# Kernel optimization log

Measured on AMD Instinct MI355X. Metric: run time of the kernel, lower is better.

The kernel has to match this reference:

```python
import jax, jax.numpy as jnp
import numpy as np

B, S, E = 2, 2048, 2048
H, D = 16, 128           # n_heads, head_dim (= rope_dim)
BASE = 10000.0


def _rope_tables(seq_len, dim):
    inv_freq = 1.0 / (BASE ** (jnp.arange(0, dim, 2, dtype=jnp.float32) / dim))
    t = jnp.arange(seq_len, dtype=jnp.float32)
    freqs = jnp.outer(t, inv_freq)                 # [S, D/2]
    emb = jnp.concatenate([freqs, freqs], axis=-1)  # [S, D]
    cos = jnp.cos(emb)[None, :, None, :]            # [1, S, 1, D]
    sin = jnp.sin(emb)[None, :, None, :]
    return cos, sin


def _rotate_half(x):
    x1, x2 = x[..., : x.shape[-1] // 2], x[..., x.shape[-1] // 2:]
    return jnp.concatenate([-x2, x1], axis=-1)


def setup_inputs() -> dict:
    key = jax.random.key(0)
    ks = jax.random.split(key, 9)
    s = 1.0 / np.sqrt(E)
    return {
        "x": jax.random.normal(ks[0], (B, S, E), dtype=jnp.float32),
        "Wq": jax.random.uniform(ks[1], (E, E), jnp.float32, -s, s),
        "bq": jax.random.uniform(ks[2], (E,), jnp.float32, -s, s),
        "Wk": jax.random.uniform(ks[3], (E, E), jnp.float32, -s, s),
        "bk": jax.random.uniform(ks[4], (E,), jnp.float32, -s, s),
        "Wv": jax.random.uniform(ks[5], (E, E), jnp.float32, -s, s),
        "bv": jax.random.uniform(ks[6], (E,), jnp.float32, -s, s),
        "Wp": jax.random.uniform(ks[7], (E, E), jnp.float32, -s, s),
        "bp": jax.random.uniform(ks[8], (E,), jnp.float32, -s, s),
    }


def reference(x, Wq, bq, Wk, bk, Wv, bv, Wp, bp):
    b, s, e = x.shape
    # QKV projections (torch Linear: y = x W^T + b)
    q = (jnp.einsum("bse,fe->bsf", x, Wq) + bq).reshape(b, s, H, D)
    k = (jnp.einsum("bse,fe->bsf", x, Wk) + bk).reshape(b, s, H, D)
    v = (jnp.einsum("bse,fe->bsf", x, Wv) + bv).reshape(b, s, H, D)
    # RoPE (rope_dim == head_dim, start_pos = 0)
    cos, sin = _rope_tables(s, D)
    q = q * cos + _rotate_half(q) * sin
    k = k * cos + _rotate_half(k) * sin
    # attention scores [b, m, n, h]
    att = jnp.einsum("bmhd,bnhd->bmnh", q, k)
    causal = jnp.tril(jnp.ones((s, s), dtype=bool))[None, :, :, None]
    att = jnp.where(causal, att, -jnp.inf)
    att = jax.nn.softmax(att / np.sqrt(D), axis=2)
    out = jnp.einsum("bmnh,bnhd->bmhd", att, v).reshape(b, s, e)
    return jnp.einsum("bse,fe->bsf", out, Wp) + bp
```

## Files before the change

### kernel.cpp

```cpp
#include <hip/hip_runtime.h>
#include <hip/hip_bf16.h>
#include <math.h>

#define BB 2
#define SS 2048
#define EE 2048
#define HH 16
#define DD 128
#define MM (BB*SS)

typedef __attribute__((ext_vector_type(8))) short bf16x8;
typedef __attribute__((ext_vector_type(4))) float f32x4;
typedef __attribute__((ext_vector_type(16))) float f32x16;
typedef __attribute__((ext_vector_type(4))) unsigned u32x4;

__device__ inline float bf2f(const __hip_bfloat16 h){ return __bfloat162float(h); }
__device__ inline __hip_bfloat16 f2bf(float f){ return __float2bfloat16(f); }
__device__ inline short f2bs(float f){
  union { __hip_bfloat16 h; short s; } u; u.h = __float2bfloat16(f); return u.s;
}
__device__ inline unsigned pk2(float a, float b){
  union { __hip_bfloat162 h2; unsigned u; } x;
  x.h2 = __float22bfloat162_rn(float2{a,b}); return x.u;
}

__device__ inline void gload16(const void* g, void* l){
  __builtin_amdgcn_global_load_lds((const __attribute__((address_space(1))) void*)g,
      (__attribute__((address_space(3))) void*)l, 16, 0, 0);
}

#define QSCL 0.12754614533018515f

__global__ void cvt_kernel(const float* __restrict__ in, __hip_bfloat16* __restrict__ out, int n4){
  int i = blockIdx.x*256 + threadIdx.x;
  if (i >= n4) return;
  float4 v = ((const float4*)in)[i];
  union { short4 s4; short s[4]; } u;
  u.s[0] = f2bs(v.x); u.s[1] = f2bs(v.y); u.s[2] = f2bs(v.z); u.s[3] = f2bs(v.w);
  ((short4*)out)[i] = u.s4;
}

struct P4 { const float* s0; const float* s1; const float* s2; const float* s3;
            __hip_bfloat16* d0; __hip_bfloat16* d1; __hip_bfloat16* d2; __hip_bfloat16* d3; };
__global__ void cvt4_kernel(P4 p, int n4){
  int w = blockIdx.y;
  const float* in = w==0 ? p.s0 : w==1 ? p.s1 : w==2 ? p.s2 : p.s3;
  __hip_bfloat16* out = w==0 ? p.d0 : w==1 ? p.d1 : w==2 ? p.d2 : p.d3;
  int i = blockIdx.x*256 + threadIdx.x;
  if (i >= n4) return;
  float4 v = ((const float4*)in)[i];
  union { short4 s4; short s[4]; } u;
  u.s[0] = f2bs(v.x); u.s[1] = f2bs(v.y); u.s[2] = f2bs(v.z); u.s[3] = f2bs(v.w);
  ((short4*)out)[i] = u.s4;
}

__global__ void rope_tables_kernel(float* __restrict__ cost, float* __restrict__ sint){
  int idx = blockIdx.x*256 + threadIdx.x;
  int s = idx >> 6, i = idx & 63;
  double inv = exp(-log(10000.0) * (double)i / 64.0);
  double f = (double)s * inv;
  cost[idx] = (float)cos(f);
  sint[idx] = (float)sin(f);
}

__global__ void rope_kernel(__hip_bfloat16* __restrict__ q, __hip_bfloat16* __restrict__ k,
                            const float* __restrict__ cost, const float* __restrict__ sint){
  int idx = blockIdx.x*256 + threadIdx.x;
  int i = idx & 63;
  int h = (idx >> 6) & (HH-1);
  int bs = idx >> 10;
  int s = bs & (SS-1);
  float c = cost[s*64 + i], sn = sint[s*64 + i];
  size_t base = ((size_t)bs*HH + h)*DD + i;
  float q1 = bf2f(q[base]), q2 = bf2f(q[base+64]);
  q[base]    = f2bf((q1*c - q2*sn)*QSCL);
  q[base+64] = f2bf((q2*c + q1*sn)*QSCL);
  float k1 = bf2f(k[base]), k2 = bf2f(k[base+64]);
  k[base]    = f2bf(k1*c - k2*sn);
  k[base+64] = f2bf(k2*c + k1*sn);
}

template<int MODE>
__global__ __launch_bounds__(512) void gemm256(const __hip_bfloat16* __restrict__ A,
        const __hip_bfloat16* __restrict__ Bw, const float* __restrict__ bias,
        void* __restrict__ Cout){
  __shared__ __align__(1024) char lds[98304];
  const int tid = threadIdx.x, wid = tid>>6, lane = tid&63, g = lane>>4, c16 = lane&15;
  const int wm = wid>>2, wn = wid&3;
  const int orig = blockIdx.x;
  const int wg = (orig & 7)*32 + (orig >> 3);
  const int bm = wg & 31, bn = wg >> 5;
  const int rowA0 = bm*128, rowB0 = bn*256;
  const char* Ab8 = (const char*)A + (size_t)rowA0*4096;
  const char* Bb8 = (const char*)Bw + (size_t)rowB0*4096;

  f32x4 acc[4][4] = {};

  auto stage = [&](int t, int b){
    char* ad = lds + b*49152;
    char* bd = lds + b*49152 + 16384;
    #pragma unroll
    for (int i=0;i<2;i++){
      int off = i*8192 + tid*16;
      int r = off >> 7;
      int cs = (off & 127) ^ ((r&7)<<4);
      gload16(Ab8 + (size_t)r*4096 + t*128 + cs, ad + i*8192 + wid*1024);
    }
    #pragma unroll
    for (int i=0;i<4;i++){
      int off = i*8192 + tid*16;
      int r = off >> 7;
      int cs = (off & 127) ^ ((r&7)<<4);
      gload16(Bb8 + (size_t)r*4096 + t*128 + cs, bd + i*8192 + wid*1024);
    }
  };

  auto compute = [&](int b){
    const char* Abuf = lds + b*49152;
    const char* Bbuf = lds + b*49152 + 16384;
    bf16x8 bfr[4][2];
    #pragma unroll
    for (int ni=0;ni<4;ni++){
      int r = wn*64 + ni*16 + c16;
      int sw = (r&7)<<4;
      #pragma unroll
      for (int kk=0;kk<2;kk++)
        bfr[ni][kk] = *(const bf16x8*)(Bbuf + r*128 + ((kk*64 + g*16) ^ sw));
    }
    #pragma unroll
    for (int mi=0;mi<4;mi++){
      int r = wm*64 + mi*16 + c16;
      int sw = (r&7)<<4;
      bf16x8 af0 = *(const bf16x8*)(Abuf + r*128 + ((g*16) ^ sw));
      bf16x8 af1 = *(const bf16x8*)(Abuf + r*128 + ((64 + g*16) ^ sw));
      __builtin_amdgcn_s_setprio(1);
      #pragma unroll
      for (int ni=0;ni<4;ni++){
        acc[mi][ni] = __builtin_amdgcn_mfma_f32_16x16x32_bf16(af0, bfr[ni][0], acc[mi][ni],0,0,0);
        acc[mi][ni] = __builtin_amdgcn_mfma_f32_16x16x32_bf16(af1, bfr[ni][1], acc[mi][ni],0,0,0);
      }
      __builtin_amdgcn_s_setprio(0);
    }
  };

  stage(0,0);
  stage(1,1);
  asm volatile("s_waitcnt vmcnt(6)" ::: "memory");
  asm volatile("s_barrier" ::: "memory");

  #pragma unroll 1
  for (int tt = 0; tt < 32; tt += 2){
    compute(0);
    asm volatile("s_barrier" ::: "memory");
    if (tt + 2 < 32){ stage(tt+2, 0); asm volatile("s_waitcnt vmcnt(6)" ::: "memory"); }
    else            {                 asm volatile("s_waitcnt vmcnt(0)" ::: "memory"); }
    asm volatile("s_barrier" ::: "memory");
    compute(1);
    if (tt + 2 < 32){
      asm volatile("s_barrier" ::: "memory");
      if (tt + 3 < 32){ stage(tt+3, 1); asm volatile("s_waitcnt vmcnt(6)" ::: "memory"); }
      else            {                 asm volatile("s_waitcnt vmcnt(0)" ::: "memory"); }
      asm volatile("s_barrier" ::: "memory");
    }
  }

  #pragma unroll
  for (int mi=0;mi<4;mi++){
    #pragma unroll
    for (int ni=0;ni<4;ni++){
      int f = rowB0 + wn*64 + ni*16 + c16;
      float bv = bias[f];
      #pragma unroll
      for (int j=0;j<4;j++){
        int m = rowA0 + wm*64 + mi*16 + g*4 + j;
        float v = acc[mi][ni][j] + bv;
        if constexpr (MODE == 0) {
          ((__hip_bfloat16*)Cout)[(size_t)m*EE + f] = f2bf(v);
        } else if constexpr (MODE == 1) {
          int b = m >> 11, s = m & (SS-1);
          ((__hip_bfloat16*)Cout)[((size_t)(b*EE + f))*SS + s] = f2bf(v);
        } else {
          ((float*)Cout)[(size_t)m*EE + f] = v;
        }
      }
    }
  }
}

__global__ __launch_bounds__(256, 2) void attn_kernel(const __hip_bfloat16* __restrict__ qg,
    const __hip_bfloat16* __restrict__ kg, const __hip_bfloat16* __restrict__ vtg,
    __hip_bfloat16* __restrict__ og){
  __shared__ short Ks[2][64*128];
  __shared__ short Vs[2][128*64];
  const int tid=threadIdx.x, wid=tid>>6, lane=tid&63;
  const int c32 = lane & 31, hi = lane >> 5;
  const int id = blockIdx.x;
  const int u = id & 255;
  const int bh = u & 31, pr = u >> 5;
  const int qtile = (id < 256) ? (15 - pr) : pr;
  const int b = bh >> 4, h = bh & 15;
  const int q0 = qtile*128, qw = q0 + wid*32;
  const int qglob = qw + c32;
  const int niter = 2*qtile + 2;

  const char* kb8 = (const char*)(kg + ((size_t)b*SS)*EE + h*DD);
  const char* vb8 = (const char*)(vtg + (size_t)bh*DD*SS);

  const char* qrow = (const char*)(qg + ((size_t)(b*SS + qglob))*EE + h*DD);
  bf16x8 qf[8];
  #pragma unroll
  for (int s=0;s<8;s++) qf[s] = *(const bf16x8*)(qrow + s*32 + hi*16);

  f32x16 pacc[4] = {};
  float mrun = -INFINITY, lrun = 0.f;

  auto stageK = [&](int kv, int buf){
    #pragma unroll
    for (int i=0;i<4;i++){
      int base = i*4096 + wid*1024;
      int lb = base + lane*16;
      int r = lb >> 8, cb = lb & 255;
      gload16(kb8 + (size_t)(kv + r)*4096 + (cb ^ ((r&7)<<4)), (char*)Ks[buf] + base);
    }
  };
  auto stageV = [&](int kv, int buf){
    #pragma unroll
    for (int i=0;i<4;i++){
      int base = i*4096 + wid*1024;
      int lb = base + lane*16;
      int d = lb >> 7, cb = lb & 127;
      gload16(vb8 + (size_t)d*4096 + (size_t)kv*2 + (cb ^ ((d&7)<<4)), (char*)Vs[buf] + base);
    }
  };

  stageK(0,0); stageV(0,0);
  __syncthreads();

  int cur = 0;
  #pragma unroll 1
  for (int it = 0; it < niter; ++it){
    const int kv0 = it*64;
    if (it + 1 < niter){ stageK(kv0+64, cur^1); stageV(kv0+64, cur^1); }

    f32x16 st0 = {}, st1 = {};
    {
      const char* Kb = (const char*)Ks[cur];
      const int sw = (c32 & 7) << 4;
      __builtin_amdgcn_s_setprio(1);
      #pragma unroll
      for (int s=0;s<8;s++){
        bf16x8 kf0 = *(const bf16x8*)(Kb + c32*256        + ((s*32 + hi*16) ^ sw));
        bf16x8 kf1 = *(const bf16x8*)(Kb + (32+c32)*256   + ((s*32 + hi*16) ^ sw));
        st0 = __builtin_amdgcn_mfma_f32_32x32x16_bf16(kf0, qf[s], st0, 0,0,0);
        st1 = __builtin_amdgcn_mfma_f32_32x32x16_bf16(kf1, qf[s], st1, 0,0,0);
      }
      __builtin_amdgcn_s_setprio(0);
    }

    float p[32];
    float vmax = -INFINITY;
    const bool domask = (kv0 + 63 > qw);
    #pragma unroll
    for (int r=0;r<16;r++){
      float v0 = st0[r], v1 = st1[r];
      if (domask){
        int kvo = (r&3) + 8*(r>>2) + 4*hi;
        if (kv0 + kvo > qglob)      v0 = -INFINITY;
        if (kv0 + 32 + kvo > qglob) v1 = -INFINITY;
      }
      p[r] = v0; p[16+r] = v1;
      vmax = fmaxf(vmax, fmaxf(v0, v1));
    }
    vmax = fmaxf(vmax, __shfl_xor(vmax, 32));

    const bool anynew = !__all(vmax <= mrun);
    float mnew = mrun;
    if (anynew){
      mnew = fmaxf(mrun, vmax);
      const float rs = exp2f(mrun - mnew);
      mrun = mnew;
      lrun *= rs;
      #pragma unroll
      for (int ds=0; ds<4; ds++)
        #pragma unroll
        for (int r=0;r<16;r++) pacc[ds][r] *= rs;
    }

    float s0=0.f, s1=0.f, s2=0.f, s3=0.f;
    #pragma unroll
    for (int i=0;i<8;i++){
      p[i]    = exp2f(p[i]    - mnew); s0 += p[i];
      p[8+i]  = exp2f(p[8+i]  - mnew); s1 += p[8+i];
      p[16+i] = exp2f(p[16+i] - mnew); s2 += p[16+i];
      p[24+i] = exp2f(p[24+i] - mnew); s3 += p[24+i];
    }
    float ps = (s0 + s1) + (s2 + s3);
    ps += __shfl_xor(ps, 32);
    lrun += ps;

    unsigned w[2][4][2];
    #pragma unroll
    for (int T=0;T<2;T++)
      #pragma unroll
      for (int m=0;m<4;m++)
        #pragma unroll
        for (int uu=0;uu<2;uu++)
          w[T][m][uu] = pk2(p[T*16 + 4*m + 2*uu], p[T*16 + 4*m + 2*uu + 1]);

    bf16x8 pf[4];
    #pragma unroll
    for (int ks=0; ks<4; ks++){
      int T = ks>>1, lo2 = (ks&1)*2;
      unsigned o0 = hi ? w[T][lo2+1][0] : w[T][lo2+0][0];
      unsigned o1 = hi ? w[T][lo2+1][1] : w[T][lo2+0][1];
      unsigned x0 = hi ? w[T][lo2+0][0] : w[T][lo2+1][0];
      unsigned x1 = hi ? w[T][lo2+0][1] : w[T][lo2+1][1];
      unsigned r0 = (unsigned)__shfl_xor((int)x0, 32);
      unsigned r1 = (unsigned)__shfl_xor((int)x1, 32);
      union { u32x4 u4; bf16x8 h8; } cvt;
      cvt.u4[0] = hi ? r0 : o0;
      cvt.u4[1] = hi ? r1 : o1;
      cvt.u4[2] = hi ? o0 : r0;
      cvt.u4[3] = hi ? o1 : r1;
      pf[ks] = cvt.h8;
    }

    {
      const char* Vb = (const char*)Vs[cur];
      const int vsw = (c32 & 7) << 4;
      __builtin_amdgcn_s_setprio(1);
      #pragma unroll
      for (int ds=0; ds<4; ds++){
        const char* vr = Vb + (ds*32 + c32)*128;
        #pragma unroll
        for (int ks=0; ks<4; ks++){
          bf16x8 vf = *(const bf16x8*)(vr + ((ks*32 + hi*16) ^ vsw));
          pacc[ds] = __builtin_amdgcn_mfma_f32_32x32x16_bf16(vf, pf[ks], pacc[ds], 0,0,0);
        }
      }
      __builtin_amdgcn_s_setprio(0);
    }

    __syncthreads();
    cur ^= 1;
  }

  const float invl = 1.0f / lrun;
  char* orow = (char*)(og + ((size_t)(b*SS + qglob))*EE + h*DD);
  #pragma unroll
  for (int ds=0; ds<4; ds++){
    #pragma unroll
    for (int m=0;m<4;m++){
      int d0 = ds*32 + 8*m + 4*hi;
      short4 s4;
      s4.x = f2bs(pacc[ds][4*m+0]*invl);
      s4.y = f2bs(pacc[ds][4*m+1]*invl);
      s4.z = f2bs(pacc[ds][4*m+2]*invl);
      s4.w = f2bs(pacc[ds][4*m+3]*invl);
      *(short4*)(orow + d0*2) = s4;
    }
  }
}

extern "C" void kernel_launch(void* const* d_in, const int* in_sizes, int n_in,
                              void* d_out, int out_size, void* d_ws, size_t ws_size,
                              hipStream_t stream){
  const float* x  = (const float*)d_in[0];
  const float* Wq = (const float*)d_in[1];
  const float* bq = (const float*)d_in[2];
  const float* Wk = (const float*)d_in[3];
  const float* bk = (const float*)d_in[4];
  const float* Wv = (const float*)d_in[5];
  const float* bv = (const float*)d_in[6];
  const float* Wp = (const float*)d_in[7];
  const float* bp = (const float*)d_in[8];
  float* out = (float*)d_out;

  char* ws = (char*)d_ws;
  size_t off = 0;
  auto alloc = [&](size_t bytes){ void* p = ws + off; off += (bytes + 255) & ~(size_t)255; return p; };
  const size_t nx = (size_t)MM*EE;
  const size_t nw = (size_t)EE*EE;
  __hip_bfloat16* xb  = (__hip_bfloat16*)alloc(nx*2);
  __hip_bfloat16* wqb = (__hip_bfloat16*)alloc(nw*2);
  __hip_bfloat16* wkb = (__hip_bfloat16*)alloc(nw*2);
  __hip_bfloat16* wvb = (__hip_bfloat16*)alloc(nw*2);
  __hip_bfloat16* wpb = (__hip_bfloat16*)alloc(nw*2);
  __hip_bfloat16* qb  = (__hip_bfloat16*)alloc(nx*2);
  __hip_bfloat16* kb  = (__hip_bfloat16*)alloc(nx*2);
  __hip_bfloat16* vtb = (__hip_bfloat16*)alloc(nx*2);
  __hip_bfloat16* ob  = (__hip_bfloat16*)alloc(nx*2);
  float* cost = (float*)alloc((size_t)SS*64*4);
  float* sint = (float*)alloc((size_t)SS*64*4);

  cvt_kernel<<<(int)(nx/4/256), 256, 0, stream>>>(x, xb, (int)(nx/4));
  P4 p4{Wq, Wk, Wv, Wp, wqb, wkb, wvb, wpb};
  cvt4_kernel<<<dim3((int)(nw/4/256), 4), 256, 0, stream>>>(p4, (int)(nw/4));
  rope_tables_kernel<<<SS*64/256, 256, 0, stream>>>(cost, sint);

  gemm256<0><<<256, 512, 0, stream>>>(xb, wqb, bq, qb);
  gemm256<0><<<256, 512, 0, stream>>>(xb, wkb, bk, kb);
  gemm256<1><<<256, 512, 0, stream>>>(xb, wvb, bv, vtb);

  rope_kernel<<<(BB*SS*HH*64)/256, 256, 0, stream>>>(qb, kb, cost, sint);

  attn_kernel<<<dim3(512), 256, 0, stream>>>(qb, kb, vtb, ob);

  gemm256<2><<<256, 512, 0, stream>>>(ob, wpb, bp, out);
}
```

Measured before the change: 288.1 us.

## Skew PV matmul by one iteration for half the waves with triple-buffered V

Waves 2 and 3 now defer their P·V MFMA by one KV iteration, running it at the start of the next iteration before the QK^T MFMA. Waves 0 and 1 keep the original order, so the two halves of the block interleave softmax work with matrix work instead of all hitting the same phase at once. V shared memory grows from double to triple buffering so the deferred read never races with the prefetch. This raises LDS use to about 80KB per block, which stays within the two-blocks-per-CU launch bound on this GPU's LDS capacity. It also adds pointer rotation and an extra tail P·V step after the loop.

```diff
diff --git a/kernel.cpp b/kernel.cpp
--- a/kernel.cpp
+++ b/kernel.cpp
@@ -191,9 +191,10 @@
     const __hip_bfloat16* __restrict__ kg, const __hip_bfloat16* __restrict__ vtg,
     __hip_bfloat16* __restrict__ og){
   __shared__ short Ks[2][64*128];
-  __shared__ short Vs[2][128*64];
+  __shared__ short Vs3[3][128*64];
   const int tid=threadIdx.x, wid=tid>>6, lane=tid&63;
   const int c32 = lane & 31, hi = lane >> 5;
+  const bool skew = (wid >= 2);
   const int id = blockIdx.x;
   const int u = id & 255;
   const int bh = u & 31, pr = u >> 5;
@@ -213,38 +214,58 @@
 
   f32x16 pacc[4] = {};
   float mrun = -INFINITY, lrun = 0.f;
-
-  auto stageK = [&](int kv, int buf){
+  bf16x8 pf[4];
+
+  auto stageK = [&](int kv, short* dst){
     #pragma unroll
     for (int i=0;i<4;i++){
       int base = i*4096 + wid*1024;
       int lb = base + lane*16;
       int r = lb >> 8, cb = lb & 255;
-      gload16(kb8 + (size_t)(kv + r)*4096 + (cb ^ ((r&7)<<4)), (char*)Ks[buf] + base);
+      gload16(kb8 + (size_t)(kv + r)*4096 + (cb ^ ((r&7)<<4)), (char*)dst + base);
     }
   };
-  auto stageV = [&](int kv, int buf){
+  auto stageV = [&](int kv, short* dst){
     #pragma unroll
     for (int i=0;i<4;i++){
       int base = i*4096 + wid*1024;
       int lb = base + lane*16;
       int d = lb >> 7, cb = lb & 127;
-      gload16(vb8 + (size_t)d*4096 + (size_t)kv*2 + (cb ^ ((d&7)<<4)), (char*)Vs[buf] + base);
+      gload16(vb8 + (size_t)d*4096 + (size_t)kv*2 + (cb ^ ((d&7)<<4)), (char*)dst + base);
     }
   };
-
-  stageK(0,0); stageV(0,0);
+  auto pvadd = [&](const short* vbuf){
+    const char* Vb = (const char*)vbuf;
+    const int vsw = (c32 & 7) << 4;
+    __builtin_amdgcn_s_setprio(1);
+    #pragma unroll
+    for (int ds=0; ds<4; ds++){
+      const char* vr = Vb + (ds*32 + c32)*128;
+      #pragma unroll
+      for (int ks=0; ks<4; ks++){
+        bf16x8 vf = *(const bf16x8*)(vr + ((ks*32 + hi*16) ^ vsw));
+        pacc[ds] = __builtin_amdgcn_mfma_f32_32x32x16_bf16(vf, pf[ks], pacc[ds], 0,0,0);
+      }
+    }
+    __builtin_amdgcn_s_setprio(0);
+  };
+
+  short* va = Vs3[0]; short* vbuf = Vs3[1]; short* vc = Vs3[2];
+  short* kc = Ks[0];  short* kn = Ks[1];
+
+  stageK(0, kc); stageV(0, vbuf);
   __syncthreads();
 
-  int cur = 0;
   #pragma unroll 1
   for (int it = 0; it < niter; ++it){
     const int kv0 = it*64;
-    if (it + 1 < niter){ stageK(kv0+64, cur^1); stageV(kv0+64, cur^1); }
+    if (it + 1 < niter){ stageK(kv0+64, kn); stageV(kv0+64, vc); }
+
+    if (skew && it > 0) pvadd(va);
 
     f32x16 st0 = {}, st1 = {};
     {
-      const char* Kb = (const char*)Ks[cur];
+      const char* Kb = (const char*)kc;
       const int sw = (c32 & 7) << 4;
       __builtin_amdgcn_s_setprio(1);
       #pragma unroll
@@ -307,7 +328,6 @@
         for (int uu=0;uu<2;uu++)
           w[T][m][uu] = pk2(p[T*16 + 4*m + 2*uu], p[T*16 + 4*m + 2*uu + 1]);
 
-    bf16x8 pf[4];
     #pragma unroll
     for (int ks=0; ks<4; ks++){
       int T = ks>>1, lo2 = (ks&1)*2;
@@ -325,25 +345,14 @@
       pf[ks] = cvt.h8;
     }
 
-    {
-      const char* Vb = (const char*)Vs[cur];
-      const int vsw = (c32 & 7) << 4;
-      __builtin_amdgcn_s_setprio(1);
-      #pragma unroll
-      for (int ds=0; ds<4; ds++){
-        const char* vr = Vb + (ds*32 + c32)*128;
-        #pragma unroll
-        for (int ks=0; ks<4; ks++){
-          bf16x8 vf = *(const bf16x8*)(vr + ((ks*32 + hi*16) ^ vsw));
-          pacc[ds] = __builtin_amdgcn_mfma_f32_32x32x16_bf16(vf, pf[ks], pacc[ds], 0,0,0);
-        }
-      }
-      __builtin_amdgcn_s_setprio(0);
-    }
+    if (!skew) pvadd(vbuf);
 
     __syncthreads();
-    cur ^= 1;
+    short* t = va; va = vbuf; vbuf = vc; vc = t;
+    short* tk = kc; kc = kn; kn = tk;
   }
+
+  if (skew) pvadd(va);
 
   const float invl = 1.0f / lrun;
   char* orow = (char*)(og + ((size_t)(b*SS + qglob))*EE + h*DD);
```

Result: faster. 275.4 us (-4.4%).
